# Kernel tuning notes

Hardware: AMD Instinct MI355X
Metric: run time of the kernel (lower is better)

## Reference

```python
import jax, jax.numpy as jnp
import numpy as np

PH, PW, PS = 4, 4, 16          # patch grid h/w and patch_size
SEQ = PS * PS                  # 256 tokens per chunk
EH = EW = ET = 4               # mem_expand_size
RPW = 2 * EW + 1               # 9
RPH = 2 * EH + 1               # 9
RPF = RPH * RPW                # 81
HEADS, DHEAD, DIM = 16, 64, 1024
INNER = HEADS * DHEAD
SCALE = DHEAD ** -0.5


def _pos(idx):
    nf = PH * PW
    inner = idx % nf
    return inner % PH, inner // PH, idx // nf


def _rotary(freqs, t):
    # freqs: [n, rot_dim] broadcast over leading dims of t [..., n, rot_dim]
    x1 = t[..., 0::2]
    x2 = t[..., 1::2]
    rot = jnp.stack((-x2, x1), axis=-1).reshape(t.shape)
    return t * jnp.cos(freqs) + rot * jnp.sin(freqs)


def setup_inputs() -> dict:
    key = jax.random.key(0)
    ks = jax.random.split(key, 9)
    B, M, TXT = 16, 8, 77
    KV = M * SEQ + TXT
    return {
        "x": jax.random.normal(ks[0], (B, SEQ, DIM), jnp.float32),
        "cond": jax.random.normal(ks[1], (B, KV, DIM), jnp.float32),
        "freqs": jax.random.normal(ks[2], (PH * PS, PW * PS, DHEAD), jnp.float32),
        "Wq": jax.random.normal(ks[3], (DIM, INNER), jnp.float32) * 0.02,
        "Wk": jax.random.normal(ks[4], (DIM, INNER), jnp.float32) * 0.02,
        "Wv": jax.random.normal(ks[5], (DIM, INNER), jnp.float32) * 0.02,
        "rel_table": jax.random.normal(ks[6], (RPH * RPW * (2 * ET + 1), HEADS), jnp.float32) * 0.02,
        "Wo": jax.random.normal(ks[7], (INNER, DIM), jnp.float32) * 0.02,
        "bo": jax.random.normal(ks[8], (DIM,), jnp.float32) * 0.02,
        "mem_idxs": jnp.arange(8, dtype=jnp.int64) if jax.config.jax_enable_x64 else jnp.arange(8, dtype=jnp.int32),
        "cur_patch_idx": 21,
    }


def reference(x, cond, freqs, Wq, Wk, Wv, rel_table, Wo, bo, mem_idxs, cur_patch_idx):
    B = x.shape[0]
    M = mem_idxs.shape[0]
    MS = M * SEQ
    # QKV projections -> [b, h, n, d]
    q = (x @ Wq).reshape(B, SEQ, HEADS, DHEAD).transpose(0, 2, 1, 3)
    k = (cond @ Wk).reshape(B, -1, HEADS, DHEAD).transpose(0, 2, 1, 3)
    v = (cond @ Wv).reshape(B, -1, HEADS, DHEAD).transpose(0, 2, 1, 3)

    # relative position indices (gather into bias table)
    rs, cs, ts = _pos(cur_patch_idx)           # python ints (static)
    rt, ct, tt = _pos(mem_idxs)                # [M] arrays
    rel_idx = (rt - rs + EH) * RPW + (ct - cs + EW) + (tt - ts + ET) * RPF
    bias = rel_table[rel_idx]                  # [M, H]
    bias = jnp.repeat(bias.T, SEQ, axis=1)[None, :, :, None]  # [1, H, M*SEQ, 1]
    km = k[:, :, :MS] + bias                   # bias added to memory K before rotary

    # rotary freqs: source patch (static slice) and target patches (gathered)
    src = freqs[rs * PS:(rs + 1) * PS, cs * PS:(cs + 1) * PS].reshape(SEQ, -1)
    rows = rt[:, None] * PS + jnp.arange(PS)   # [M, PS]
    cols = ct[:, None] * PS + jnp.arange(PS)   # [M, PS]
    tgt = freqs[rows[:, :, None], cols[:, None, :]].reshape(MS, -1)  # [M*SEQ, rot]

    q = _rotary(src, q)
    km = _rotary(tgt, km)
    k = jnp.concatenate([km, k[:, :, MS:]], axis=2)

    dots = jnp.einsum('bhid,bhjd->bhij', q, k) * SCALE
    attn = jax.nn.softmax(dots, axis=-1)
    out = jnp.einsum('bhij,bhjd->bhid', attn, v)
    out = out.transpose(0, 2, 1, 3).reshape(B, SEQ, INNER)
    return out @ Wo + bo
```

## Files before the change

### kernel.cpp

```cpp
#include <hip/hip_runtime.h>
#include <cstdint>

typedef __bf16 bf16;
typedef bf16 bf16x2 __attribute__((ext_vector_type(2)));
typedef bf16 bf16x4 __attribute__((ext_vector_type(4)));
typedef bf16 bf16x8 __attribute__((ext_vector_type(8)));
typedef float floatx4 __attribute__((ext_vector_type(4)));

#define SEQ   256
#define DIMM  1024
#define HEADS 16
#define KV_LEN 2125
#define KV_PAD 2176
#define KV_BLKS 17
#define MS_TOK 2048
#define ATT_SCALE 0.125f
#define TILE_ELEMS (128 * 32)

__device__ __forceinline__ void load_lds16(const bf16* g, bf16* l) {
    __builtin_amdgcn_global_load_lds(
        (const __attribute__((address_space(1))) void*)g,
        (__attribute__((address_space(3))) void*)l, 16, 0, 0);
}

__global__ __launch_bounds__(256) void convert_kernel(
        const float* __restrict__ src, bf16* __restrict__ dst, long total) {
    long i4 = ((long)blockIdx.x * 256 + threadIdx.x) * 4;
    if (i4 >= total) return;
    const float4 v = *(const float4*)(src + i4);
    bf16x4 o;
    o[0] = (bf16)v.x; o[1] = (bf16)v.y; o[2] = (bf16)v.z; o[3] = (bf16)v.w;
    *(bf16x4*)(dst + i4) = o;
}

__global__ __launch_bounds__(256) void convert_cond_kernel(
        const float* __restrict__ src, bf16* __restrict__ dst, long total_dst) {
    long i4 = ((long)blockIdx.x * 256 + threadIdx.x) * 4;
    if (i4 >= total_dst) return;
    long drow = i4 >> 10;
    int b = (int)(drow / KV_PAD);
    int j = (int)(drow - (long)b * KV_PAD);
    bf16x4 o;
    if (j < KV_LEN) {
        long srow = (long)b * KV_LEN + j;
        const float4 v = *(const float4*)(src + (srow << 10) + (i4 & 1023));
        o[0] = (bf16)v.x; o[1] = (bf16)v.y; o[2] = (bf16)v.z; o[3] = (bf16)v.w;
    } else {
        o[0] = o[1] = o[2] = o[3] = (bf16)0.f;
    }
    *(bf16x4*)(dst + i4) = o;
}

__global__ __launch_bounds__(256) void transpose_bf16_kernel(
        const float* __restrict__ W, bf16* __restrict__ Wt, int N) {
    __shared__ float tile[32][33];
    int n0 = blockIdx.x * 32, k0 = blockIdx.y * 32;
    int r = threadIdx.x >> 5, c = threadIdx.x & 31;
    #pragma unroll
    for (int i = 0; i < 4; ++i)
        tile[r + i * 8][c] = W[(size_t)(k0 + r + i * 8) * N + n0 + c];
    __syncthreads();
    #pragma unroll
    for (int i = 0; i < 4; ++i)
        Wt[(size_t)(n0 + r + i * 8) * N + k0 + c] = (bf16)tile[c][r + i * 8];
}

__global__ __launch_bounds__(256) void rot_tables_kernel(
        const float* __restrict__ freqs, const float* __restrict__ rel_table,
        const int* __restrict__ mem_idxs, const int* __restrict__ cur,
        float* __restrict__ ckT, float* __restrict__ skT,
        float* __restrict__ cqT, float* __restrict__ sqT,
        float* __restrict__ biasK) {
    int t = blockIdx.x * 256 + threadIdx.x;
    const int cp = *cur; const int inner = cp & 15;
    const int rs = inner & 3, cs = inner >> 2, ts = cp >> 4;
    if (t < MS_TOK * 64) {
        int j = t >> 6, d = t & 63;
        int mi = mem_idxs[j >> 8];
        int rt = mi & 3, ct = (mi >> 2) & 3;
        int pidx = j & 255;
        int fr = rt * 16 + (pidx >> 4), fc = ct * 16 + (pidx & 15);
        float f = freqs[(size_t)(fr * 64 + fc) * 64 + d];
        ckT[t] = __cosf(f); skT[t] = __sinf(f);
    } else if (t < MS_TOK * 64 + SEQ * 64) {
        int t2 = t - MS_TOK * 64;
        int s = t2 >> 6, d = t2 & 63;
        int fr = rs * 16 + (s >> 4), fc = cs * 16 + (s & 15);
        float f = freqs[(size_t)(fr * 64 + fc) * 64 + d];
        cqT[t2] = __cosf(f); sqT[t2] = __sinf(f);
    } else if (t < MS_TOK * 64 + SEQ * 64 + 128) {
        int t3 = t - (MS_TOK * 64 + SEQ * 64);
        int m = t3 >> 4, h = t3 & 15;
        int mi = mem_idxs[m];
        int rt = mi & 3, ct = (mi >> 2) & 3, tt = mi >> 4;
        int rel = (rt - rs + 4) * 9 + (ct - cs + 4) + (tt - ts + 4) * 81;
        biasK[t3] = rel_table[rel * HEADS + h];
    }
}

__device__ __forceinline__ void gemm_loop_db(
        const bf16* __restrict__ Ag, const bf16* __restrict__ Bg, int K,
        bf16* __restrict__ As, bf16* __restrict__ Bs,
        floatx4 (&acc)[4][4]) {
    const int tid  = threadIdx.x;
    const int wave = tid >> 6, lane = tid & 63;
    const int quad = lane >> 4, l16 = lane & 15;
    const int wm = wave >> 1, wn = wave & 1;
    #pragma unroll
    for (int i = 0; i < 2; ++i) {
        int c = i * 256 + wave * 64 + lane;
        int r = c >> 2, c8 = (c & 3) * 8;
        load_lds16(Ag + (long)r * K + c8, As + (i * 256 + wave * 64) * 8);
        load_lds16(Bg + (long)r * K + c8, Bs + (i * 256 + wave * 64) * 8);
    }
    for (int k0 = 0; k0 < K; k0 += 32) {
        const int cur = (k0 >> 5) & 1;
        bf16* Asc = As + cur * TILE_ELEMS;
        bf16* Bsc = Bs + cur * TILE_ELEMS;
        __syncthreads();
        if (k0 + 32 < K) {
            bf16* Asn = As + (cur ^ 1) * TILE_ELEMS;
            bf16* Bsn = Bs + (cur ^ 1) * TILE_ELEMS;
            #pragma unroll
            for (int i = 0; i < 2; ++i) {
                int c = i * 256 + wave * 64 + lane;
                int r = c >> 2, c8 = (c & 3) * 8;
                load_lds16(Ag + (long)r * K + k0 + 32 + c8, Asn + (i * 256 + wave * 64) * 8);
                load_lds16(Bg + (long)r * K + k0 + 32 + c8, Bsn + (i * 256 + wave * 64) * 8);
            }
        }
        bf16x8 af[4], bfr[4];
        #pragma unroll
        for (int mt = 0; mt < 4; ++mt)
            af[mt] = *(const bf16x8*)(Asc + (wm * 64 + mt * 16 + l16) * 32 + quad * 8);
        #pragma unroll
        for (int nt = 0; nt < 4; ++nt)
            bfr[nt] = *(const bf16x8*)(Bsc + (wn * 64 + nt * 16 + l16) * 32 + quad * 8);
        #pragma unroll
        for (int mt = 0; mt < 4; ++mt)
            #pragma unroll
            for (int nt = 0; nt < 4; ++nt)
                acc[mt][nt] = __builtin_amdgcn_mfma_f32_16x16x32_bf16(af[mt], bfr[nt], acc[mt][nt], 0, 0, 0);
    }
}

__global__ __launch_bounds__(256) void gemm_o_kernel(
        const bf16* __restrict__ A, const bf16* __restrict__ Bt,
        float* __restrict__ Cout, const float* __restrict__ bias, int N) {
    __shared__ bf16 As[2 * TILE_ELEMS];
    __shared__ bf16 Bs[2 * TILE_ELEMS];
    const int tid  = threadIdx.x;
    const int wave = tid >> 6, lane = tid & 63;
    const int quad = lane >> 4, l16 = lane & 15;
    const int wm = wave >> 1, wn = wave & 1;
    const int L = blockIdx.x, xcd = L & 7, ii = L >> 3;
    const long row0 = (long)(xcd * 4 + (ii >> 3)) * 128;
    const long col0 = (long)(ii & 7) * 128;
    floatx4 acc[4][4] = {};
    gemm_loop_db(A + row0 * DIMM, Bt + col0 * DIMM, DIMM, As, Bs, acc);
    #pragma unroll
    for (int mt = 0; mt < 4; ++mt) {
        #pragma unroll
        for (int nt = 0; nt < 4; ++nt) {
            long r = row0 + wm * 64 + mt * 16 + quad * 4;
            long ccol = col0 + wn * 64 + nt * 16 + l16;
            float bv = bias[ccol];
            #pragma unroll
            for (int i = 0; i < 4; ++i)
                Cout[(r + i) * (long)N + ccol] = acc[mt][nt][i] + bv;
        }
    }
}

__global__ __launch_bounds__(256) void gemm_q_rot_kernel(
        const bf16* __restrict__ A, const bf16* __restrict__ Bt,
        bf16* __restrict__ Qout, const float* __restrict__ cqT,
        const float* __restrict__ sqT) {
    __shared__ bf16 As[2 * TILE_ELEMS];
    __shared__ bf16 Bs[2 * TILE_ELEMS];
    const int tid  = threadIdx.x;
    const int wave = tid >> 6, lane = tid & 63;
    const int quad = lane >> 4, l16 = lane & 15;
    const int wm = wave >> 1, wn = wave & 1;
    const int L = blockIdx.x, xcd = L & 7, ii = L >> 3;
    const long row0 = (long)(xcd * 4 + (ii >> 3)) * 128;
    const long col0 = (long)(ii & 7) * 128;
    floatx4 acc[4][4] = {};
    gemm_loop_db(A + row0 * DIMM, Bt + col0 * DIMM, DIMM, As, Bs, acc);
    #pragma unroll
    for (int mt = 0; mt < 4; ++mt) {
        #pragma unroll
        for (int nt = 0; nt < 4; ++nt) {
            long rr = row0 + wm * 64 + mt * 16 + quad * 4;
            int ccol = (int)col0 + wn * 64 + nt * 16 + l16;
            int d = ccol & 63;
            #pragma unroll
            for (int i = 0; i < 4; ++i) {
                long r = rr + i; int s = (int)(r & 255);
                float c_ = cqT[s * 64 + d], s_ = sqT[s * 64 + d];
                float q = acc[mt][nt][i];
                float pn = __shfl_xor(q, 1);
                float outv = (d & 1) ? (q * c_ + pn * s_) : (q * c_ - pn * s_);
                Qout[r * DIMM + ccol] = (bf16)outv;
            }
        }
    }
}

__global__ __launch_bounds__(256) void gemm_k_kernel(
        const bf16* __restrict__ A, const bf16* __restrict__ Btk,
        bf16* __restrict__ Kout, const float* __restrict__ ckT,
        const float* __restrict__ skT, const float* __restrict__ biasK) {
    __shared__ bf16 As[2 * TILE_ELEMS];
    __shared__ bf16 Bs[2 * TILE_ELEMS];
    const int tid  = threadIdx.x;
    const int wave = tid >> 6, lane = tid & 63;
    const int quad = lane >> 4, l16 = lane & 15;
    const int wm = wave >> 1, wn = wave & 1;
    const int L = blockIdx.x, xcd = L & 7, ii = L >> 3;
    const long row0 = (long)(xcd * 34 + (ii >> 3)) * 128;
    const long col0 = (long)(ii & 7) * 128;
    floatx4 acc[4][4] = {};
    gemm_loop_db(A + row0 * DIMM, Btk + col0 * DIMM, DIMM, As, Bs, acc);
    const int bidx = (int)(row0 / KV_PAD);
    #pragma unroll
    for (int mt = 0; mt < 4; ++mt) {
        #pragma unroll
        for (int nt = 0; nt < 4; ++nt) {
            long rr = row0 + wm * 64 + mt * 16 + quad * 4;
            int ccol = (int)col0 + wn * 64 + nt * 16 + l16;
            int h = ccol >> 6, d = ccol & 63;
            int jbase = (int)(rr - (long)bidx * KV_PAD);
            #pragma unroll
            for (int i = 0; i < 4; ++i) {
                int j = jbase + i;
                float kb = acc[mt][nt][i];
                float c_ = 1.f, s_ = 0.f;
                if (j < MS_TOK) {
                    kb += biasK[((j >> 8) << 4) + h];
                    c_ = ckT[j * 64 + d]; s_ = skT[j * 64 + d];
                }
                float pn = __shfl_xor(kb, 1);
                float outv = (d & 1) ? (kb * c_ + pn * s_) : (kb * c_ - pn * s_);
                Kout[(rr + i) * DIMM + ccol] = (bf16)outv;
            }
        }
    }
}

__global__ __launch_bounds__(256) void gemm_vt_kernel(
        const bf16* __restrict__ Wvt, const bf16* __restrict__ condb,
        bf16* __restrict__ VT) {
    __shared__ bf16 As[2 * TILE_ELEMS];
    __shared__ bf16 Bs[2 * TILE_ELEMS];
    const int tid  = threadIdx.x;
    const int wave = tid >> 6, lane = tid & 63;
    const int quad = lane >> 4, l16 = lane & 15;
    const int wm = wave >> 1, wn = wave & 1;
    const int L = blockIdx.x, xcd = L & 7, ii = L >> 3;
    const int pan = xcd * 34 + (ii >> 3);
    const int b  = pan / KV_BLKS, tb = pan % KV_BLKS;
    const long row0 = (long)(ii & 7) * 128;
    const long col0 = (long)tb * 128;
    const bf16* Bt = condb + (size_t)b * KV_PAD * DIMM;
    floatx4 acc[4][4] = {};
    gemm_loop_db(Wvt + row0 * DIMM, Bt + col0 * DIMM, DIMM, As, Bs, acc);
    #pragma unroll
    for (int mt = 0; mt < 4; ++mt) {
        #pragma unroll
        for (int nt = 0; nt < 4; ++nt) {
            long f0 = row0 + wm * 64 + mt * 16 + quad * 4;
            long t0 = col0 + wn * 64 + nt * 16 + l16;
            #pragma unroll
            for (int i = 0; i < 4; ++i)
                VT[((size_t)b * DIMM + f0 + i) * KV_PAD + t0] = (bf16)acc[mt][nt][i];
        }
    }
}

__global__ __launch_bounds__(256, 3) void attn_kernel(
        const bf16* __restrict__ Qb, const bf16* __restrict__ Kb,
        const bf16* __restrict__ VT, bf16* __restrict__ Ob) {
    const int L = blockIdx.x, xcd = L & 7, ii = L >> 3;
    const int bh = xcd * 32 + (ii >> 2), qt = ii & 3;
    const int b = bh >> 4, h = bh & 15;
    const int tid = threadIdx.x, wave = tid >> 6, lane = tid & 63;
    const int quad = lane >> 4, l16 = lane & 15;
    __shared__ bf16 Ks[128 * 72];
    __shared__ bf16 Vt[64 * 144];
    __shared__ bf16 Ps[4][16 * 72];

    const int qrow0 = b * SEQ + qt * 64 + wave * 16;
    const bf16* qp = Qb + (size_t)(qrow0 + l16) * DIMM + h * 64 + quad * 8;
    bf16x8 qf0 = *(const bf16x8*)(qp);
    bf16x8 qf1 = *(const bf16x8*)(qp + 32);

    floatx4 oacc[4] = {};
    floatx4 lacc = {};
    bf16x8 ones;
    #pragma unroll
    for (int t = 0; t < 8; ++t) ones[t] = (bf16)1.0f;

    const size_t kbase = ((size_t)b * KV_PAD) * DIMM + h * 64;
    const size_t vbase = ((size_t)(bh * 64)) * KV_PAD;

    const int kchunk = tid & 1;
    const int gl = tid >> 1;
    const int g  = ((gl & 31) << 2) | (gl >> 5);
    const int gg = g & 63;
    const int dstrow = (g >> 6) * 64 + ((gg & 3) << 4) + (gg >> 2);
    const int vd = tid >> 2, vseg = tid & 3;

    bf16x8 kr[4], vr[4];
    {
        int jr = g; if (jr > KV_LEN - 1) jr = KV_LEN - 1;
        const bf16* gp = Kb + kbase + (size_t)jr * DIMM + kchunk * 32;
        kr[0] = *(const bf16x8*)(gp);      kr[1] = *(const bf16x8*)(gp + 8);
        kr[2] = *(const bf16x8*)(gp + 16); kr[3] = *(const bf16x8*)(gp + 24);
        const bf16* vp = VT + vbase + (size_t)vd * KV_PAD + vseg * 32;
        vr[0] = *(const bf16x8*)(vp);      vr[1] = *(const bf16x8*)(vp + 8);
        vr[2] = *(const bf16x8*)(vp + 16); vr[3] = *(const bf16x8*)(vp + 24);
    }

    for (int j0 = 0; j0 < KV_LEN; j0 += 128) {
        __syncthreads();
        {
            bf16* dp = Ks + dstrow * 72 + kchunk * 32;
            *(bf16x8*)(dp)      = kr[0]; *(bf16x8*)(dp + 8)  = kr[1];
            *(bf16x8*)(dp + 16) = kr[2]; *(bf16x8*)(dp + 24) = kr[3];
            bf16* dv = Vt + vd * 144 + vseg * 32;
            *(bf16x8*)(dv)      = vr[0]; *(bf16x8*)(dv + 8)  = vr[1];
            *(bf16x8*)(dv + 16) = vr[2]; *(bf16x8*)(dv + 24) = vr[3];
        }
        __syncthreads();
        if (j0 + 128 < KV_LEN) {
            int jr = j0 + 128 + g; if (jr > KV_LEN - 1) jr = KV_LEN - 1;
            const bf16* gp = Kb + kbase + (size_t)jr * DIMM + kchunk * 32;
            kr[0] = *(const bf16x8*)(gp);      kr[1] = *(const bf16x8*)(gp + 8);
            kr[2] = *(const bf16x8*)(gp + 16); kr[3] = *(const bf16x8*)(gp + 24);
            const bf16* vp = VT + vbase + (size_t)vd * KV_PAD + j0 + 128 + vseg * 32;
            vr[0] = *(const bf16x8*)(vp);      vr[1] = *(const bf16x8*)(vp + 8);
            vr[2] = *(const bf16x8*)(vp + 16); vr[3] = *(const bf16x8*)(vp + 24);
        }
        #pragma unroll
        for (int c = 0; c < 2; ++c) {
            floatx4 s[4] = {};
            #pragma unroll
            for (int jt = 0; jt < 4; ++jt) {
                const bf16* kp = Ks + (c * 64 + jt * 16 + l16) * 72 + quad * 8;
                bf16x8 kb0 = *(const bf16x8*)(kp);
                bf16x8 kb1 = *(const bf16x8*)(kp + 32);
                s[jt] = __builtin_amdgcn_mfma_f32_16x16x32_bf16(qf0, kb0, s[jt], 0, 0, 0);
                s[jt] = __builtin_amdgcn_mfma_f32_16x16x32_bf16(qf1, kb1, s[jt], 0, 0, 0);
            }
            const int colbase = j0 + c * 64 + 4 * l16;
            #pragma unroll
            for (int r = 0; r < 4; ++r) {
                bf16x4 pk;
                #pragma unroll
                for (int jt = 0; jt < 4; ++jt) {
                    bool ok = (colbase + jt) < KV_LEN;
                    float p = ok ? __expf(s[jt][r] * ATT_SCALE) : 0.f;
                    pk[jt] = (bf16)p;
                }
                *(bf16x4*)(&Ps[wave][(quad * 4 + r) * 72 + l16 * 4]) = pk;
            }
            #pragma unroll
            for (int kf = 0; kf < 2; ++kf) {
                bf16x8 pa = *(const bf16x8*)(&Ps[wave][l16 * 72 + kf * 32 + quad * 8]);
                lacc = __builtin_amdgcn_mfma_f32_16x16x32_bf16(pa, ones, lacc, 0, 0, 0);
                #pragma unroll
                for (int dt = 0; dt < 4; ++dt) {
                    bf16x8 vb = *(const bf16x8*)(Vt + (dt * 16 + l16) * 144 + c * 64 + kf * 32 + quad * 8);
                    oacc[dt] = __builtin_amdgcn_mfma_f32_16x16x32_bf16(pa, vb, oacc[dt], 0, 0, 0);
                }
            }
        }
    }
    #pragma unroll
    for (int r = 0; r < 4; ++r) {
        float inv = 1.f / lacc[r];
        size_t orow = (size_t)(qrow0 + quad * 4 + r) * DIMM + h * 64;
        #pragma unroll
        for (int dt = 0; dt < 4; ++dt)
            Ob[orow + dt * 16 + l16] = (bf16)(oacc[dt][r] * inv);
    }
}

extern "C" void kernel_launch(void* const* d_in, const int* in_sizes, int n_in,
                              void* d_out, int out_size, void* d_ws, size_t ws_size,
                              hipStream_t stream) {
    const float* x     = (const float*)d_in[0];
    const float* cond  = (const float*)d_in[1];
    const float* freqs = (const float*)d_in[2];
    const float* Wq    = (const float*)d_in[3];
    const float* Wk    = (const float*)d_in[4];
    const float* Wv    = (const float*)d_in[5];
    const float* rel   = (const float*)d_in[6];
    const float* Wo    = (const float*)d_in[7];
    const float* bo    = (const float*)d_in[8];
    const int* mem_idxs = (const int*)d_in[9];
    const int* cur      = (const int*)d_in[10];
    float* out = (float*)d_out;

    const int B   = 16;
    const int Mq  = B * SEQ;
    const int Mkv_pad = B * KV_PAD;

    char* ws = (char*)d_ws;
    size_t off = 0;
    auto alloc = [&](size_t bytes) { void* pp = ws + off; off = (off + bytes + 255) & ~(size_t)255; return pp; };
    bf16* xb    = (bf16*)alloc((size_t)Mq * DIMM * 2);
    bf16* condb = (bf16*)alloc((size_t)Mkv_pad * DIMM * 2);
    bf16* Wqt   = (bf16*)alloc((size_t)DIMM * DIMM * 2);
    bf16* Wkt   = (bf16*)alloc((size_t)DIMM * DIMM * 2);
    bf16* Wvt   = (bf16*)alloc((size_t)DIMM * DIMM * 2);
    bf16* Wot   = (bf16*)alloc((size_t)DIMM * DIMM * 2);
    bf16* Qb    = (bf16*)alloc((size_t)Mq * DIMM * 2);
    bf16* Kb    = (bf16*)alloc((size_t)Mkv_pad * DIMM * 2);
    bf16* VTb   = (bf16*)alloc((size_t)B * DIMM * KV_PAD * 2);
    bf16* Ab    = (bf16*)alloc((size_t)Mq * DIMM * 2);
    float* ckT  = (float*)alloc((size_t)MS_TOK * 64 * 4);
    float* skT  = (float*)alloc((size_t)MS_TOK * 64 * 4);
    float* cqT  = (float*)alloc((size_t)SEQ * 64 * 4);
    float* sqT  = (float*)alloc((size_t)SEQ * 64 * 4);
    float* biasK = (float*)alloc(128 * 4);

    long xtot = (long)Mq * DIMM;
    convert_kernel<<<(int)((xtot / 4 + 255) / 256), 256, 0, stream>>>(x, xb, xtot);
    long ctot = (long)Mkv_pad * DIMM;
    convert_cond_kernel<<<(int)((ctot / 4 + 255) / 256), 256, 0, stream>>>(cond, condb, ctot);
    dim3 tg(32, 32);
    transpose_bf16_kernel<<<tg, 256, 0, stream>>>(Wq, Wqt, DIMM);
    transpose_bf16_kernel<<<tg, 256, 0, stream>>>(Wk, Wkt, DIMM);
    transpose_bf16_kernel<<<tg, 256, 0, stream>>>(Wv, Wvt, DIMM);
    transpose_bf16_kernel<<<tg, 256, 0, stream>>>(Wo, Wot, DIMM);

    int ttot = MS_TOK * 64 + SEQ * 64 + 128;
    rot_tables_kernel<<<(ttot + 255) / 256, 256, 0, stream>>>(
        freqs, rel, mem_idxs, cur, ckT, skT, cqT, sqT, biasK);

    gemm_q_rot_kernel<<<256, 256, 0, stream>>>(xb, Wqt, Qb, cqT, sqT);
    gemm_k_kernel<<<2176, 256, 0, stream>>>(condb, Wkt, Kb, ckT, skT, biasK);
    gemm_vt_kernel<<<2176, 256, 0, stream>>>(Wvt, condb, VTb);

    attn_kernel<<<1024, 256, 0, stream>>>(Qb, Kb, VTb, Ab);

    gemm_o_kernel<<<256, 256, 0, stream>>>(Ab, Wot, out, bo, DIMM);
}
```

Baseline: 590.3 us.

## Use 256x256-tile, 4-stage pipelined GEMM core for K and V projections

Replaces the 128x128 double-buffered GEMM used by the K and V^T projection kernels with a 256x256 tile core run by 8 waves. It adds a 4-slot LDS ring filled by direct global-to-LDS loads with explicit vmcnt waits, an XOR swizzle on the LDS layout, split compute phases and s_setprio around the MFMA bursts. The aim is more data reuse per tile and better overlap of loads with matrix math on the two largest GEMMs. In exchange each block uses about 128KB of LDS, which limits occupancy to one block per CU. The V^T grid also reads padded columns past KV_PAD for the last batch, while its stores are guarded.

```diff
diff --git a/kernel.cpp b/kernel.cpp
--- a/kernel.cpp
+++ b/kernel.cpp
@@ -16,6 +16,7 @@
 #define MS_TOK 2048
 #define ATT_SCALE 0.125f
 #define TILE_ELEMS (128 * 32)
+#define SLOT_ELEMS (256 * 32)
 
 __device__ __forceinline__ void load_lds16(const bf16* g, bf16* l) {
     __builtin_amdgcn_global_load_lds(
@@ -144,6 +145,94 @@
     }
 }
 
+#define VMW8 asm volatile("s_waitcnt vmcnt(8)" ::: "memory")
+#define VMW4 asm volatile("s_waitcnt vmcnt(4)" ::: "memory")
+#define VMW0 asm volatile("s_waitcnt vmcnt(0)" ::: "memory")
+#define VMNONE
+
+#define TILE_PHASES(t, DO_STAGE, WAITOP)                                        \
+  {                                                                             \
+    const int slot_ = (t) & 3;                                                  \
+    const bf16* Asl = As + slot_ * SLOT_ELEMS;                                  \
+    const bf16* Bsl = Bs + slot_ * SLOT_ELEMS;                                  \
+    bf16x8 bfr[4], afr[4];                                                      \
+    _Pragma("unroll")                                                           \
+    for (int n = 0; n < 4; ++n)                                                 \
+      bfr[n] = *(const bf16x8*)(Bsl + boff + n * 512);                          \
+    _Pragma("unroll")                                                           \
+    for (int m = 0; m < 4; ++m)                                                 \
+      afr[m] = *(const bf16x8*)(Asl + aoff + m * 512);                          \
+    if (DO_STAGE) { stageA((t) + 3); }                                          \
+    __builtin_amdgcn_s_barrier();                                               \
+    __builtin_amdgcn_sched_barrier(0);                                          \
+    __builtin_amdgcn_s_setprio(1);                                              \
+    _Pragma("unroll")                                                           \
+    for (int m = 0; m < 4; ++m)                                                 \
+      _Pragma("unroll")                                                         \
+      for (int n = 0; n < 4; ++n)                                               \
+        acc[m][n] = __builtin_amdgcn_mfma_f32_16x16x32_bf16(afr[m], bfr[n], acc[m][n], 0, 0, 0); \
+    __builtin_amdgcn_s_setprio(0);                                              \
+    __builtin_amdgcn_s_barrier();                                               \
+    __builtin_amdgcn_sched_barrier(0);                                          \
+    _Pragma("unroll")                                                           \
+    for (int m = 0; m < 4; ++m)                                                 \
+      afr[m] = *(const bf16x8*)(Asl + aoff + 2048 + m * 512);                   \
+    if (DO_STAGE) { stageB((t) + 3); }                                          \
+    __builtin_amdgcn_s_barrier();                                               \
+    __builtin_amdgcn_sched_barrier(0);                                          \
+    __builtin_amdgcn_s_setprio(1);                                              \
+    _Pragma("unroll")                                                           \
+    for (int m = 0; m < 4; ++m)                                                 \
+      _Pragma("unroll")                                                         \
+      for (int n = 0; n < 4; ++n)                                               \
+        acc[m + 4][n] = __builtin_amdgcn_mfma_f32_16x16x32_bf16(afr[m], bfr[n], acc[m + 4][n], 0, 0, 0); \
+    __builtin_amdgcn_s_setprio(0);                                              \
+    WAITOP;                                                                     \
+    __builtin_amdgcn_s_barrier();                                               \
+    __builtin_amdgcn_sched_barrier(0);                                          \
+  }
+
+__device__ __forceinline__ void gemm256_core(
+        const bf16* __restrict__ Ag, const bf16* __restrict__ Bg,
+        bf16* __restrict__ As, bf16* __restrict__ Bs,
+        floatx4 (&acc)[8][4]) {
+    const int tid  = threadIdx.x;
+    const int wave = tid >> 6, lane = tid & 63;
+    const int quad = lane >> 4, l16 = lane & 15;
+    const int wm = wave >> 2, wn = wave & 3;
+    const int p0 = tid, p1 = 512 + tid;
+    const int r0 = p0 >> 2, s0 = (p0 & 3) ^ ((r0 >> 1) & 3);
+    const int r1 = p1 >> 2, s1 = (p1 & 3) ^ ((r1 >> 1) & 3);
+    const long oS0 = (long)r0 * DIMM + s0 * 8;
+    const long oS1 = (long)r1 * DIMM + s1 * 8;
+    const int dU0 = (wave * 64) * 8;
+    const int dU1 = (512 + wave * 64) * 8;
+    auto stageA = [&](int kt) {
+        bf16* dst = As + (kt & 3) * SLOT_ELEMS;
+        load_lds16(Ag + oS0 + kt * 32, dst + dU0);
+        load_lds16(Ag + oS1 + kt * 32, dst + dU1);
+    };
+    auto stageB = [&](int kt) {
+        bf16* dst = Bs + (kt & 3) * SLOT_ELEMS;
+        load_lds16(Bg + oS0 + kt * 32, dst + dU0);
+        load_lds16(Bg + oS1 + kt * 32, dst + dU1);
+    };
+    const int xterm = (quad ^ ((l16 >> 1) & 3)) * 8;
+    const int aoff = (wm * 128 + l16) * 32 + xterm;
+    const int boff = (wn * 64 + l16) * 32 + xterm;
+
+    stageA(0); stageB(0); stageA(1); stageB(1); stageA(2); stageB(2);
+    VMW8;
+    __builtin_amdgcn_s_barrier();
+    __builtin_amdgcn_sched_barrier(0);
+
+    for (int t = 0; t < 29; ++t)
+        TILE_PHASES(t, true, VMW8)
+    TILE_PHASES(29, false, VMW4)
+    TILE_PHASES(30, false, VMW0)
+    TILE_PHASES(31, false, VMNONE)
+}
+
 __global__ __launch_bounds__(256) void gemm_o_kernel(
         const bf16* __restrict__ A, const bf16* __restrict__ Bt,
         float* __restrict__ Cout, const float* __restrict__ bias, int N) {
@@ -207,30 +296,31 @@
     }
 }
 
-__global__ __launch_bounds__(256) void gemm_k_kernel(
+__global__ __launch_bounds__(512, 2) void gemm_k_kernel(
         const bf16* __restrict__ A, const bf16* __restrict__ Btk,
         bf16* __restrict__ Kout, const float* __restrict__ ckT,
         const float* __restrict__ skT, const float* __restrict__ biasK) {
-    __shared__ bf16 As[2 * TILE_ELEMS];
-    __shared__ bf16 Bs[2 * TILE_ELEMS];
+    __shared__ bf16 As[4 * SLOT_ELEMS];
+    __shared__ bf16 Bs[4 * SLOT_ELEMS];
     const int tid  = threadIdx.x;
     const int wave = tid >> 6, lane = tid & 63;
     const int quad = lane >> 4, l16 = lane & 15;
-    const int wm = wave >> 1, wn = wave & 1;
-    const int L = blockIdx.x, xcd = L & 7, ii = L >> 3;
-    const long row0 = (long)(xcd * 34 + (ii >> 3)) * 128;
-    const long col0 = (long)(ii & 7) * 128;
-    floatx4 acc[4][4] = {};
-    gemm_loop_db(A + row0 * DIMM, Btk + col0 * DIMM, DIMM, As, Bs, acc);
-    const int bidx = (int)(row0 / KV_PAD);
-    #pragma unroll
-    for (int mt = 0; mt < 4; ++mt) {
+    const int wm = wave >> 2, wn = wave & 3;
+    const int L = (int)blockIdx.x;
+    const int logical = (L & 7) * 68 + (L >> 3);
+    const long row0 = (long)(logical >> 2) * 256;
+    const long col0 = (long)(logical & 3) * 256;
+    floatx4 acc[8][4] = {};
+    gemm256_core(A + row0 * DIMM, Btk + col0 * DIMM, As, Bs, acc);
+    #pragma unroll
+    for (int mt = 0; mt < 8; ++mt) {
         #pragma unroll
         for (int nt = 0; nt < 4; ++nt) {
-            long rr = row0 + wm * 64 + mt * 16 + quad * 4;
+            int rr = (int)row0 + wm * 128 + mt * 16 + quad * 4;
             int ccol = (int)col0 + wn * 64 + nt * 16 + l16;
             int h = ccol >> 6, d = ccol & 63;
-            int jbase = (int)(rr - (long)bidx * KV_PAD);
+            int bidx = rr / KV_PAD;
+            int jbase = rr - bidx * KV_PAD;
             #pragma unroll
             for (int i = 0; i < 4; ++i) {
                 int j = jbase + i;
@@ -242,38 +332,41 @@
                 }
                 float pn = __shfl_xor(kb, 1);
                 float outv = (d & 1) ? (kb * c_ + pn * s_) : (kb * c_ - pn * s_);
-                Kout[(rr + i) * DIMM + ccol] = (bf16)outv;
-            }
-        }
-    }
-}
-
-__global__ __launch_bounds__(256) void gemm_vt_kernel(
+                Kout[(long)(rr + i) * DIMM + ccol] = (bf16)outv;
+            }
+        }
+    }
+}
+
+__global__ __launch_bounds__(512, 2) void gemm_vt_kernel(
         const bf16* __restrict__ Wvt, const bf16* __restrict__ condb,
         bf16* __restrict__ VT) {
-    __shared__ bf16 As[2 * TILE_ELEMS];
-    __shared__ bf16 Bs[2 * TILE_ELEMS];
+    __shared__ bf16 As[4 * SLOT_ELEMS];
+    __shared__ bf16 Bs[4 * SLOT_ELEMS];
     const int tid  = threadIdx.x;
     const int wave = tid >> 6, lane = tid & 63;
     const int quad = lane >> 4, l16 = lane & 15;
-    const int wm = wave >> 1, wn = wave & 1;
-    const int L = blockIdx.x, xcd = L & 7, ii = L >> 3;
-    const int pan = xcd * 34 + (ii >> 3);
-    const int b  = pan / KV_BLKS, tb = pan % KV_BLKS;
-    const long row0 = (long)(ii & 7) * 128;
-    const long col0 = (long)tb * 128;
+    const int wm = wave >> 2, wn = wave & 3;
+    const int L = (int)blockIdx.x;
+    const int logical = (L & 7) * 72 + (L >> 3);
+    const int b = logical / 36, i36 = logical % 36;
+    const long row0 = (long)(i36 & 3) * 256;
+    const long col0 = (long)(i36 >> 2) * 256;
     const bf16* Bt = condb + (size_t)b * KV_PAD * DIMM;
-    floatx4 acc[4][4] = {};
-    gemm_loop_db(Wvt + row0 * DIMM, Bt + col0 * DIMM, DIMM, As, Bs, acc);
-    #pragma unroll
-    for (int mt = 0; mt < 4; ++mt) {
+    floatx4 acc[8][4] = {};
+    gemm256_core(Wvt + row0 * DIMM, Bt + col0 * DIMM, As, Bs, acc);
+    #pragma unroll
+    for (int mt = 0; mt < 8; ++mt) {
         #pragma unroll
         for (int nt = 0; nt < 4; ++nt) {
-            long f0 = row0 + wm * 64 + mt * 16 + quad * 4;
-            long t0 = col0 + wn * 64 + nt * 16 + l16;
-            #pragma unroll
-            for (int i = 0; i < 4; ++i)
-                VT[((size_t)b * DIMM + f0 + i) * KV_PAD + t0] = (bf16)acc[mt][nt][i];
+            int tfrag = (int)col0 + wn * 64 + nt * 16;
+            if (tfrag < KV_PAD) {
+                long f0 = row0 + wm * 128 + mt * 16 + quad * 4;
+                long t0 = tfrag + l16;
+                #pragma unroll
+                for (int i = 0; i < 4; ++i)
+                    VT[((size_t)b * DIMM + f0 + i) * KV_PAD + t0] = (bf16)acc[mt][nt][i];
+            }
         }
     }
 }
@@ -441,8 +534,8 @@
         freqs, rel, mem_idxs, cur, ckT, skT, cqT, sqT, biasK);
 
     gemm_q_rot_kernel<<<256, 256, 0, stream>>>(xb, Wqt, Qb, cqT, sqT);
-    gemm_k_kernel<<<2176, 256, 0, stream>>>(condb, Wkt, Kb, ckT, skT, biasK);
-    gemm_vt_kernel<<<2176, 256, 0, stream>>>(Wvt, condb, VTb);
+    gemm_k_kernel<<<544, 512, 0, stream>>>(condb, Wkt, Kb, ckT, skT, biasK);
+    gemm_vt_kernel<<<576, 512, 0, stream>>>(Wvt, condb, VTb);
 
     attn_kernel<<<1024, 256, 0, stream>>>(Qb, Kb, VTb, Ab);
 
```

Measured after the change: 679.0 us. 1.15x slower.

## Use 4-slot LDS ring with XOR swizzle and explicit vmcnt waits in GEMMs

Applied to the files above, without the earlier changes.

Replaces the double-buffered GEMM main loop with a 4-slot LDS ring that prefetches three k-tiles ahead. The loop is fully unrolled with explicit s_waitcnt vmcnt and raw s_barrier calls, so each iteration waits only for the tile it needs rather than syncing on all outstanding loads. An XOR swizzle on the 16-byte column chunk is meant to reduce LDS bank conflicts on fragment reads. LDS per block doubles to 64KB, launch bounds now ask for 2 blocks per CU, and K is hardcoded to 1024.

```diff
diff --git a/kernel.cpp b/kernel.cpp
--- a/kernel.cpp
+++ b/kernel.cpp
@@ -15,7 +15,7 @@
 #define KV_BLKS 17
 #define MS_TOK 2048
 #define ATT_SCALE 0.125f
-#define TILE_ELEMS (128 * 32)
+#define SLOT128 (128 * 32)
 
 __device__ __forceinline__ void load_lds16(const bf16* g, bf16* l) {
     __builtin_amdgcn_global_load_lds(
@@ -98,57 +98,78 @@
     }
 }
 
-__device__ __forceinline__ void gemm_loop_db(
-        const bf16* __restrict__ Ag, const bf16* __restrict__ Bg, int K,
+#define VMW8 asm volatile("s_waitcnt vmcnt(8)" ::: "memory")
+#define VMW4 asm volatile("s_waitcnt vmcnt(4)" ::: "memory")
+#define VMW0 asm volatile("s_waitcnt vmcnt(0)" ::: "memory")
+#define VMNONE
+
+#define R4_BODY(t, DO_STAGE, WAITOP)                                          \
+  {                                                                           \
+    const bf16* Asl = As + ((t) & 3) * SLOT128;                               \
+    const bf16* Bsl = Bs + ((t) & 3) * SLOT128;                               \
+    if (DO_STAGE) stage((t) + 3);                                             \
+    bf16x8 af[4], bfr[4];                                                     \
+    _Pragma("unroll")                                                         \
+    for (int mt = 0; mt < 4; ++mt)                                            \
+      af[mt] = *(const bf16x8*)(Asl + aoff + mt * 512);                       \
+    _Pragma("unroll")                                                         \
+    for (int nt = 0; nt < 4; ++nt)                                            \
+      bfr[nt] = *(const bf16x8*)(Bsl + boff + nt * 512);                      \
+    _Pragma("unroll")                                                         \
+    for (int mt = 0; mt < 4; ++mt)                                            \
+      _Pragma("unroll")                                                       \
+      for (int nt = 0; nt < 4; ++nt)                                          \
+        acc[mt][nt] = __builtin_amdgcn_mfma_f32_16x16x32_bf16(af[mt], bfr[nt], acc[mt][nt], 0, 0, 0); \
+    WAITOP;                                                                   \
+    __builtin_amdgcn_s_barrier();                                             \
+    __builtin_amdgcn_sched_barrier(0);                                        \
+  }
+
+__device__ __forceinline__ void gemm_loop_r4(
+        const bf16* __restrict__ Ag, const bf16* __restrict__ Bg,
         bf16* __restrict__ As, bf16* __restrict__ Bs,
         floatx4 (&acc)[4][4]) {
     const int tid  = threadIdx.x;
     const int wave = tid >> 6, lane = tid & 63;
     const int quad = lane >> 4, l16 = lane & 15;
     const int wm = wave >> 1, wn = wave & 1;
-    #pragma unroll
-    for (int i = 0; i < 2; ++i) {
-        int c = i * 256 + wave * 64 + lane;
-        int r = c >> 2, c8 = (c & 3) * 8;
-        load_lds16(Ag + (long)r * K + c8, As + (i * 256 + wave * 64) * 8);
-        load_lds16(Bg + (long)r * K + c8, Bs + (i * 256 + wave * 64) * 8);
-    }
-    for (int k0 = 0; k0 < K; k0 += 32) {
-        const int cur = (k0 >> 5) & 1;
-        bf16* Asc = As + cur * TILE_ELEMS;
-        bf16* Bsc = Bs + cur * TILE_ELEMS;
-        __syncthreads();
-        if (k0 + 32 < K) {
-            bf16* Asn = As + (cur ^ 1) * TILE_ELEMS;
-            bf16* Bsn = Bs + (cur ^ 1) * TILE_ELEMS;
-            #pragma unroll
-            for (int i = 0; i < 2; ++i) {
-                int c = i * 256 + wave * 64 + lane;
-                int r = c >> 2, c8 = (c & 3) * 8;
-                load_lds16(Ag + (long)r * K + k0 + 32 + c8, Asn + (i * 256 + wave * 64) * 8);
-                load_lds16(Bg + (long)r * K + k0 + 32 + c8, Bsn + (i * 256 + wave * 64) * 8);
-            }
-        }
-        bf16x8 af[4], bfr[4];
-        #pragma unroll
-        for (int mt = 0; mt < 4; ++mt)
-            af[mt] = *(const bf16x8*)(Asc + (wm * 64 + mt * 16 + l16) * 32 + quad * 8);
-        #pragma unroll
-        for (int nt = 0; nt < 4; ++nt)
-            bfr[nt] = *(const bf16x8*)(Bsc + (wn * 64 + nt * 16 + l16) * 32 + quad * 8);
-        #pragma unroll
-        for (int mt = 0; mt < 4; ++mt)
-            #pragma unroll
-            for (int nt = 0; nt < 4; ++nt)
-                acc[mt][nt] = __builtin_amdgcn_mfma_f32_16x16x32_bf16(af[mt], bfr[nt], acc[mt][nt], 0, 0, 0);
-    }
-}
-
-__global__ __launch_bounds__(256) void gemm_o_kernel(
+    const int p0 = tid, p1 = 256 + tid;
+    const int r0 = p0 >> 2, s0 = (p0 & 3) ^ ((r0 >> 1) & 3);
+    const int r1 = p1 >> 2, s1 = (p1 & 3) ^ ((r1 >> 1) & 3);
+    const long oS0 = (long)r0 * DIMM + s0 * 8;
+    const long oS1 = (long)r1 * DIMM + s1 * 8;
+    const int dU0 = (wave * 64) * 8;
+    const int dU1 = (256 + wave * 64) * 8;
+    auto stage = [&](int kt) {
+        bf16* da = As + (kt & 3) * SLOT128;
+        bf16* db = Bs + (kt & 3) * SLOT128;
+        const long ko = (long)kt * 32;
+        load_lds16(Ag + oS0 + ko, da + dU0);
+        load_lds16(Ag + oS1 + ko, da + dU1);
+        load_lds16(Bg + oS0 + ko, db + dU0);
+        load_lds16(Bg + oS1 + ko, db + dU1);
+    };
+    const int xterm = (quad ^ ((l16 >> 1) & 3)) * 8;
+    const int aoff = (wm * 64 + l16) * 32 + xterm;
+    const int boff = (wn * 64 + l16) * 32 + xterm;
+
+    stage(0); stage(1); stage(2);
+    VMW8;
+    __builtin_amdgcn_s_barrier();
+    __builtin_amdgcn_sched_barrier(0);
+
+    for (int t = 0; t < 29; ++t)
+        R4_BODY(t, true, VMW8)
+    R4_BODY(29, false, VMW4)
+    R4_BODY(30, false, VMW0)
+    R4_BODY(31, false, VMNONE)
+}
+
+__global__ __launch_bounds__(256, 2) void gemm_o_kernel(
         const bf16* __restrict__ A, const bf16* __restrict__ Bt,
         float* __restrict__ Cout, const float* __restrict__ bias, int N) {
-    __shared__ bf16 As[2 * TILE_ELEMS];
-    __shared__ bf16 Bs[2 * TILE_ELEMS];
+    __shared__ bf16 As[4 * SLOT128];
+    __shared__ bf16 Bs[4 * SLOT128];
     const int tid  = threadIdx.x;
     const int wave = tid >> 6, lane = tid & 63;
     const int quad = lane >> 4, l16 = lane & 15;
@@ -157,7 +178,7 @@
     const long row0 = (long)(xcd * 4 + (ii >> 3)) * 128;
     const long col0 = (long)(ii & 7) * 128;
     floatx4 acc[4][4] = {};
-    gemm_loop_db(A + row0 * DIMM, Bt + col0 * DIMM, DIMM, As, Bs, acc);
+    gemm_loop_r4(A + row0 * DIMM, Bt + col0 * DIMM, As, Bs, acc);
     #pragma unroll
     for (int mt = 0; mt < 4; ++mt) {
         #pragma unroll
@@ -172,12 +193,12 @@
     }
 }
 
-__global__ __launch_bounds__(256) void gemm_q_rot_kernel(
+__global__ __launch_bounds__(256, 2) void gemm_q_rot_kernel(
         const bf16* __restrict__ A, const bf16* __restrict__ Bt,
         bf16* __restrict__ Qout, const float* __restrict__ cqT,
         const float* __restrict__ sqT) {
-    __shared__ bf16 As[2 * TILE_ELEMS];
-    __shared__ bf16 Bs[2 * TILE_ELEMS];
+    __shared__ bf16 As[4 * SLOT128];
+    __shared__ bf16 Bs[4 * SLOT128];
     const int tid  = threadIdx.x;
     const int wave = tid >> 6, lane = tid & 63;
     const int quad = lane >> 4, l16 = lane & 15;
@@ -186,7 +207,7 @@
     const long row0 = (long)(xcd * 4 + (ii >> 3)) * 128;
     const long col0 = (long)(ii & 7) * 128;
     floatx4 acc[4][4] = {};
-    gemm_loop_db(A + row0 * DIMM, Bt + col0 * DIMM, DIMM, As, Bs, acc);
+    gemm_loop_r4(A + row0 * DIMM, Bt + col0 * DIMM, As, Bs, acc);
     #pragma unroll
     for (int mt = 0; mt < 4; ++mt) {
         #pragma unroll
@@ -207,12 +228,12 @@
     }
 }
 
-__global__ __launch_bounds__(256) void gemm_k_kernel(
+__global__ __launch_bounds__(256, 2) void gemm_k_kernel(
         const bf16* __restrict__ A, const bf16* __restrict__ Btk,
         bf16* __restrict__ Kout, const float* __restrict__ ckT,
         const float* __restrict__ skT, const float* __restrict__ biasK) {
-    __shared__ bf16 As[2 * TILE_ELEMS];
-    __shared__ bf16 Bs[2 * TILE_ELEMS];
+    __shared__ bf16 As[4 * SLOT128];
+    __shared__ bf16 Bs[4 * SLOT128];
     const int tid  = threadIdx.x;
     const int wave = tid >> 6, lane = tid & 63;
     const int quad = lane >> 4, l16 = lane & 15;
@@ -221,7 +242,7 @@
     const long row0 = (long)(xcd * 34 + (ii >> 3)) * 128;
     const long col0 = (long)(ii & 7) * 128;
     floatx4 acc[4][4] = {};
-    gemm_loop_db(A + row0 * DIMM, Btk + col0 * DIMM, DIMM, As, Bs, acc);
+    gemm_loop_r4(A + row0 * DIMM, Btk + col0 * DIMM, As, Bs, acc);
     const int bidx = (int)(row0 / KV_PAD);
     #pragma unroll
     for (int mt = 0; mt < 4; ++mt) {
@@ -248,11 +269,11 @@
     }
 }
 
-__global__ __launch_bounds__(256) void gemm_vt_kernel(
+__global__ __launch_bounds__(256, 2) void gemm_vt_kernel(
         const bf16* __restrict__ Wvt, const bf16* __restrict__ condb,
         bf16* __restrict__ VT) {
-    __shared__ bf16 As[2 * TILE_ELEMS];
-    __shared__ bf16 Bs[2 * TILE_ELEMS];
+    __shared__ bf16 As[4 * SLOT128];
+    __shared__ bf16 Bs[4 * SLOT128];
     const int tid  = threadIdx.x;
     const int wave = tid >> 6, lane = tid & 63;
     const int quad = lane >> 4, l16 = lane & 15;
@@ -264,7 +285,7 @@
     const long col0 = (long)tb * 128;
     const bf16* Bt = condb + (size_t)b * KV_PAD * DIMM;
     floatx4 acc[4][4] = {};
-    gemm_loop_db(Wvt + row0 * DIMM, Bt + col0 * DIMM, DIMM, As, Bs, acc);
+    gemm_loop_r4(Wvt + row0 * DIMM, Bt + col0 * DIMM, As, Bs, acc);
     #pragma unroll
     for (int mt = 0; mt < 4; ++mt) {
         #pragma unroll
```

Measured after the change: 654.1 us. +10.8%, slower.

## Use 256x128 tiles with swizzled LDS for K and V projection GEMMs

Applied to the files above, without the earlier changes.

Adds a 256x128 double-buffered GEMM main loop with an XOR-swizzled LDS layout and switches the K and V^T projection kernels to it, halving their grid size. Each wave now computes an 8x4 MFMA tile, so more accumulation work is done per LDS fragment load and less global traffic is spent per output. The swizzle is meant to cut LDS bank conflicts. The cost is higher register use (launch bounds 2 blocks per CU) and fewer blocks to spread across the CUs.

```diff
diff --git a/kernel.cpp b/kernel.cpp
--- a/kernel.cpp
+++ b/kernel.cpp
@@ -16,6 +16,8 @@
 #define MS_TOK 2048
 #define ATT_SCALE 0.125f
 #define TILE_ELEMS (128 * 32)
+#define SLOT_A (256 * 32)
+#define SLOT_B (128 * 32)
 
 __device__ __forceinline__ void load_lds16(const bf16* g, bf16* l) {
     __builtin_amdgcn_global_load_lds(
@@ -144,6 +146,60 @@
     }
 }
 
+__device__ __forceinline__ void gemm_loop_256x128(
+        const bf16* __restrict__ Ag, const bf16* __restrict__ Bg,
+        bf16* __restrict__ As, bf16* __restrict__ Bs,
+        floatx4 (&acc)[8][4]) {
+    const int tid  = threadIdx.x;
+    const int wave = tid >> 6, lane = tid & 63;
+    const int quad = lane >> 4, l16 = lane & 15;
+    const int wm = wave >> 1, wn = wave & 1;
+
+    auto stageA = [&](bf16* dst, int k0) {
+        #pragma unroll
+        for (int p = 0; p < 4; ++p) {
+            int c = p * 256 + tid;
+            int r = c >> 2, ch = (c & 3) ^ ((r >> 1) & 3);
+            load_lds16(Ag + (long)r * DIMM + ch * 8 + k0, dst + (p * 256 + wave * 64) * 8);
+        }
+    };
+    auto stageB = [&](bf16* dst, int k0) {
+        #pragma unroll
+        for (int p = 0; p < 2; ++p) {
+            int c = p * 256 + tid;
+            int r = c >> 2, ch = (c & 3) ^ ((r >> 1) & 3);
+            load_lds16(Bg + (long)r * DIMM + ch * 8 + k0, dst + (p * 256 + wave * 64) * 8);
+        }
+    };
+    const int xterm = (quad ^ ((l16 >> 1) & 3)) * 8;
+    const int aoff = (wm * 128 + l16) * 32 + xterm;
+    const int boff = (wn * 64 + l16) * 32 + xterm;
+
+    stageA(As, 0); stageB(Bs, 0);
+    for (int k0 = 0; k0 < DIMM; k0 += 32) {
+        const int cur = (k0 >> 5) & 1;
+        const bf16* Asc = As + cur * SLOT_A;
+        const bf16* Bsc = Bs + cur * SLOT_B;
+        __syncthreads();
+        if (k0 + 32 < DIMM) {
+            stageA(As + (cur ^ 1) * SLOT_A, k0 + 32);
+            stageB(Bs + (cur ^ 1) * SLOT_B, k0 + 32);
+        }
+        bf16x8 af[8], bfr[4];
+        #pragma unroll
+        for (int nt = 0; nt < 4; ++nt)
+            bfr[nt] = *(const bf16x8*)(Bsc + boff + nt * 512);
+        #pragma unroll
+        for (int mt = 0; mt < 8; ++mt)
+            af[mt] = *(const bf16x8*)(Asc + aoff + mt * 512);
+        #pragma unroll
+        for (int mt = 0; mt < 8; ++mt)
+            #pragma unroll
+            for (int nt = 0; nt < 4; ++nt)
+                acc[mt][nt] = __builtin_amdgcn_mfma_f32_16x16x32_bf16(af[mt], bfr[nt], acc[mt][nt], 0, 0, 0);
+    }
+}
+
 __global__ __launch_bounds__(256) void gemm_o_kernel(
         const bf16* __restrict__ A, const bf16* __restrict__ Bt,
         float* __restrict__ Cout, const float* __restrict__ bias, int N) {
@@ -207,30 +263,30 @@
     }
 }
 
-__global__ __launch_bounds__(256) void gemm_k_kernel(
+__global__ __launch_bounds__(256, 2) void gemm_k_kernel(
         const bf16* __restrict__ A, const bf16* __restrict__ Btk,
         bf16* __restrict__ Kout, const float* __restrict__ ckT,
         const float* __restrict__ skT, const float* __restrict__ biasK) {
-    __shared__ bf16 As[2 * TILE_ELEMS];
-    __shared__ bf16 Bs[2 * TILE_ELEMS];
+    __shared__ bf16 As[2 * SLOT_A];
+    __shared__ bf16 Bs[2 * SLOT_B];
     const int tid  = threadIdx.x;
     const int wave = tid >> 6, lane = tid & 63;
     const int quad = lane >> 4, l16 = lane & 15;
     const int wm = wave >> 1, wn = wave & 1;
     const int L = blockIdx.x, xcd = L & 7, ii = L >> 3;
-    const long row0 = (long)(xcd * 34 + (ii >> 3)) * 128;
+    const long row0 = (long)(xcd * 17 + (ii >> 3)) * 256;
     const long col0 = (long)(ii & 7) * 128;
-    floatx4 acc[4][4] = {};
-    gemm_loop_db(A + row0 * DIMM, Btk + col0 * DIMM, DIMM, As, Bs, acc);
-    const int bidx = (int)(row0 / KV_PAD);
-    #pragma unroll
-    for (int mt = 0; mt < 4; ++mt) {
+    floatx4 acc[8][4] = {};
+    gemm_loop_256x128(A + row0 * DIMM, Btk + col0 * DIMM, As, Bs, acc);
+    #pragma unroll
+    for (int mt = 0; mt < 8; ++mt) {
         #pragma unroll
         for (int nt = 0; nt < 4; ++nt) {
-            long rr = row0 + wm * 64 + mt * 16 + quad * 4;
+            int rr = (int)row0 + wm * 128 + mt * 16 + quad * 4;
             int ccol = (int)col0 + wn * 64 + nt * 16 + l16;
             int h = ccol >> 6, d = ccol & 63;
-            int jbase = (int)(rr - (long)bidx * KV_PAD);
+            int bidx = rr / KV_PAD;
+            int jbase = rr - bidx * KV_PAD;
             #pragma unroll
             for (int i = 0; i < 4; ++i) {
                 int j = jbase + i;
@@ -242,34 +298,34 @@
                 }
                 float pn = __shfl_xor(kb, 1);
                 float outv = (d & 1) ? (kb * c_ + pn * s_) : (kb * c_ - pn * s_);
-                Kout[(rr + i) * DIMM + ccol] = (bf16)outv;
+                Kout[(long)(rr + i) * DIMM + ccol] = (bf16)outv;
             }
         }
     }
 }
 
-__global__ __launch_bounds__(256) void gemm_vt_kernel(
+__global__ __launch_bounds__(256, 2) void gemm_vt_kernel(
         const bf16* __restrict__ Wvt, const bf16* __restrict__ condb,
         bf16* __restrict__ VT) {
-    __shared__ bf16 As[2 * TILE_ELEMS];
-    __shared__ bf16 Bs[2 * TILE_ELEMS];
+    __shared__ bf16 As[2 * SLOT_A];
+    __shared__ bf16 Bs[2 * SLOT_B];
     const int tid  = threadIdx.x;
     const int wave = tid >> 6, lane = tid & 63;
     const int quad = lane >> 4, l16 = lane & 15;
     const int wm = wave >> 1, wn = wave & 1;
     const int L = blockIdx.x, xcd = L & 7, ii = L >> 3;
-    const int pan = xcd * 34 + (ii >> 3);
+    const int pan = xcd * 34 + (ii >> 2);
     const int b  = pan / KV_BLKS, tb = pan % KV_BLKS;
-    const long row0 = (long)(ii & 7) * 128;
+    const long row0 = (long)(ii & 3) * 256;
     const long col0 = (long)tb * 128;
     const bf16* Bt = condb + (size_t)b * KV_PAD * DIMM;
-    floatx4 acc[4][4] = {};
-    gemm_loop_db(Wvt + row0 * DIMM, Bt + col0 * DIMM, DIMM, As, Bs, acc);
-    #pragma unroll
-    for (int mt = 0; mt < 4; ++mt) {
+    floatx4 acc[8][4] = {};
+    gemm_loop_256x128(Wvt + row0 * DIMM, Bt + col0 * DIMM, As, Bs, acc);
+    #pragma unroll
+    for (int mt = 0; mt < 8; ++mt) {
         #pragma unroll
         for (int nt = 0; nt < 4; ++nt) {
-            long f0 = row0 + wm * 64 + mt * 16 + quad * 4;
+            long f0 = row0 + wm * 128 + mt * 16 + quad * 4;
             long t0 = col0 + wn * 64 + nt * 16 + l16;
             #pragma unroll
             for (int i = 0; i < 4; ++i)
@@ -441,8 +497,8 @@
         freqs, rel, mem_idxs, cur, ckT, skT, cqT, sqT, biasK);
 
     gemm_q_rot_kernel<<<256, 256, 0, stream>>>(xb, Wqt, Qb, cqT, sqT);
-    gemm_k_kernel<<<2176, 256, 0, stream>>>(condb, Wkt, Kb, ckT, skT, biasK);
-    gemm_vt_kernel<<<2176, 256, 0, stream>>>(Wvt, condb, VTb);
+    gemm_k_kernel<<<1088, 256, 0, stream>>>(condb, Wkt, Kb, ckT, skT, biasK);
+    gemm_vt_kernel<<<1088, 256, 0, stream>>>(Wvt, condb, VTb);
 
     attn_kernel<<<1024, 256, 0, stream>>>(Qb, Kb, VTb, Ab);
 
```

Measured after the change: 664.6 us. 1.13x slower.
